# Kernel tuning notes

Hardware: AMD Instinct MI355X
Metric: run time of the kernel (lower is better)

Reference implementation:

```python
import jax, jax.numpy as jnp
import numpy as np

N_NODES = 50000
N_EDGES = 800000
N_LABEL = 200000
IN_DIM = 64
HID = 64
NEG_SLOPE = 0.2  # PyG GATConv default
EPS = 1e-16      # PyG softmax denominator eps


def _gat_conv(x, edge_index, edge_attr, W, att_src, att_dst, We, att_edge, bias):
    """PyG GATConv, heads=1, concat=True, add_self_loops=False, edge_dim=1."""
    n = x.shape[0]
    h = x @ W  # [N, H]
    src, dst = edge_index[0], edge_index[1]
    # per-edge attention logits
    alpha = (h @ att_src)[src] + (h @ att_dst)[dst] + (edge_attr @ We) @ att_edge  # [E]
    alpha = jax.nn.leaky_relu(alpha, NEG_SLOPE)
    # softmax over incoming edges of each dst node
    amax = jax.ops.segment_max(alpha, dst, num_segments=n)
    p = jnp.exp(alpha - amax[dst])
    denom = jax.ops.segment_sum(p, dst, num_segments=n)
    coef = p / (denom[dst] + EPS)  # [E]
    # weighted scatter-aggregate of source features
    out = jax.ops.segment_sum(h[src] * coef[:, None], dst, num_segments=n)
    return out + bias


def setup_inputs() -> dict:
    key = jax.random.key(0)
    ks = jax.random.split(key, 20)
    s = 0.05
    inp = {
        "x": jax.random.normal(ks[0], (N_NODES, IN_DIM), dtype=jnp.float32),
        "edge_attr": jax.random.normal(ks[1], (N_EDGES, 1), dtype=jnp.float32),
        "author_W": jax.random.normal(ks[2], (IN_DIM, HID), dtype=jnp.float32) * s,
        "author_b": jnp.zeros((HID,), dtype=jnp.float32),
        "c1_W": jax.random.normal(ks[3], (HID, HID), dtype=jnp.float32) * s,
        "c1_as": jax.random.normal(ks[4], (HID,), dtype=jnp.float32) * s,
        "c1_ad": jax.random.normal(ks[5], (HID,), dtype=jnp.float32) * s,
        "c1_We": jax.random.normal(ks[6], (1, HID), dtype=jnp.float32) * s,
        "c1_ae": jax.random.normal(ks[7], (HID,), dtype=jnp.float32) * s,
        "c1_b": jnp.zeros((HID,), dtype=jnp.float32),
        "c2_W": jax.random.normal(ks[8], (HID, HID), dtype=jnp.float32) * s,
        "c2_as": jax.random.normal(ks[9], (HID,), dtype=jnp.float32) * s,
        "c2_ad": jax.random.normal(ks[10], (HID,), dtype=jnp.float32) * s,
        "c2_We": jax.random.normal(ks[11], (1, HID), dtype=jnp.float32) * s,
        "c2_ae": jax.random.normal(ks[12], (HID,), dtype=jnp.float32) * s,
        "c2_b": jnp.zeros((HID,), dtype=jnp.float32),
        "edge_index": jax.random.randint(ks[13], (2, N_EDGES), 0, N_NODES, dtype=jnp.int32),
        "edge_label_index": jax.random.randint(ks[14], (2, N_LABEL), 0, N_NODES, dtype=jnp.int32),
    }
    return inp


def reference(x, edge_attr, author_W, author_b,
              c1_W, c1_as, c1_ad, c1_We, c1_ae, c1_b,
              c2_W, c2_as, c2_ad, c2_We, c2_ae, c2_b,
              edge_index, edge_label_index):
    h = x @ author_W + author_b                                   # author_lin
    h = jax.nn.relu(_gat_conv(h, edge_index, edge_attr,
                              c1_W, c1_as, c1_ad, c1_We, c1_ae, c1_b))
    h = _gat_conv(h, edge_index, edge_attr,
                  c2_W, c2_as, c2_ad, c2_We, c2_ae, c2_b)
    # edge-wise dot-product classifier
    return (h[edge_label_index[0]] * h[edge_label_index[1]]).sum(axis=-1)
```

## Files before the change

### kernel.cpp

```cpp
#include <hip/hip_runtime.h>

#define N_NODES 50000
#define N_EDGES 800000
#define N_LABEL 200000
#define HID 64
#define SCAN_BLOCKS 196
#define NBKT 196
#define NBLK 391

static const size_t OFF_W1C  = 0;
static const size_t OFF_B1C  = 4096;
static const size_t OFF_CE   = 4160;
static const size_t OFF_H    = 4224;
static const size_t OFF_AGG  = OFF_H    + (size_t)N_NODES * HID;
static const size_t OFF_ASRC = OFF_AGG  + (size_t)N_NODES * HID;
static const size_t OFF_ADST = OFF_ASRC + (size_t)N_NODES;
static const size_t OFF_ROW  = OFF_ADST + (size_t)N_NODES;
static const size_t OFF_CNT  = OFF_ROW  + (size_t)N_NODES + 2;
static const size_t OFF_PACK = OFF_CNT  + (size_t)N_NODES;
static const size_t OFF_BSUM = OFF_PACK + 2 * (size_t)N_EDGES;
static const size_t OFF_CM   = OFF_BSUM + 256;
static const size_t OFF_OM   = OFF_CM   + (size_t)NBKT * NBLK;

__global__ void prep_kernel(const float* __restrict__ Wa, const float* __restrict__ ba,
                            const float* __restrict__ c1W,
                            const float* __restrict__ c1We, const float* __restrict__ c1ae,
                            const float* __restrict__ c2We, const float* __restrict__ c2ae,
                            float* __restrict__ W1c, float* __restrict__ b1c,
                            float* __restrict__ ce) {
    int t = threadIdx.x;
    for (int idx = t; idx < 64 * 64; idx += 256) {
        int i = idx >> 6, j = idx & 63;
        float s = 0.f;
        for (int k = 0; k < 64; ++k) s += Wa[i * 64 + k] * c1W[k * 64 + j];
        W1c[idx] = s;
    }
    if (t < 64) {
        float s = 0.f;
        for (int k = 0; k < 64; ++k) s += ba[k] * c1W[k * 64 + t];
        b1c[t] = s;
    }
    if (t == 64) {
        float s = 0.f;
        for (int k = 0; k < 64; ++k) s += c1We[k] * c1ae[k];
        ce[0] = s;
    }
    if (t == 65) {
        float s = 0.f;
        for (int k = 0; k < 64; ++k) s += c2We[k] * c2ae[k];
        ce[1] = s;
    }
}

__global__ void hist_kernel(const int* __restrict__ ei, int* __restrict__ cnt) {
    int e = blockIdx.x * blockDim.x + threadIdx.x;
    if (e < N_EDGES) atomicAdd(&cnt[ei[N_EDGES + e]], 1);
}

__global__ void block_sum_kernel(const int* __restrict__ cnt, int* __restrict__ bsum) {
    __shared__ int red[256];
    int t = threadIdx.x;
    int i = blockIdx.x * 256 + t;
    red[t] = (i < N_NODES) ? cnt[i] : 0;
    __syncthreads();
    for (int off = 128; off > 0; off >>= 1) {
        if (t < off) red[t] += red[t + off];
        __syncthreads();
    }
    if (t == 0) bsum[blockIdx.x] = red[0];
}

__global__ void scan_bsum_kernel(int* __restrict__ bsum) {
    __shared__ int s[256];
    int t = threadIdx.x;
    int v = (t < SCAN_BLOCKS) ? bsum[t] : 0;
    s[t] = v;
    __syncthreads();
    for (int off = 1; off < 256; off <<= 1) {
        int u = (t >= off) ? s[t - off] : 0;
        __syncthreads();
        s[t] += u;
        __syncthreads();
    }
    if (t < SCAN_BLOCKS) bsum[t] = s[t] - v;
}

__global__ void scan_final_kernel(const int* __restrict__ cnt,
                                  const int* __restrict__ bsum,
                                  int* __restrict__ row_ptr) {
    __shared__ int s[256];
    int t = threadIdx.x;
    int i = blockIdx.x * 256 + t;
    int v = (i < N_NODES) ? cnt[i] : 0;
    s[t] = v;
    __syncthreads();
    for (int off = 1; off < 256; off <<= 1) {
        int u = (t >= off) ? s[t - off] : 0;
        __syncthreads();
        s[t] += u;
        __syncthreads();
    }
    int excl = s[t] - v + bsum[blockIdx.x];
    if (i < N_NODES) row_ptr[i] = excl;
    if (i == N_NODES - 1) row_ptr[N_NODES] = excl + v;
}

__global__ void blkhist_kernel(const int* __restrict__ ei, int* __restrict__ countM) {
    __shared__ int lh[NBKT];
    int t = threadIdx.x, blk = blockIdx.x;
    if (t < NBKT) lh[t] = 0;
    __syncthreads();
    int base = blk * 2048;
#pragma unroll
    for (int i = 0; i < 8; ++i) {
        int e = base + i * 256 + t;
        if (e < N_EDGES) atomicAdd(&lh[ei[N_EDGES + e] >> 8], 1);
    }
    __syncthreads();
    if (t < NBKT) countM[t * NBLK + blk] = lh[t];
}

__global__ void bucket_scan_kernel(const int* __restrict__ countM,
                                   const int* __restrict__ row_ptr,
                                   int* __restrict__ offM) {
    __shared__ int s[256];
    int b = blockIdx.x, t = threadIdx.x;
    int i0 = 2 * t, i1 = 2 * t + 1;
    int c0 = (i0 < NBLK) ? countM[b * NBLK + i0] : 0;
    int c1 = (i1 < NBLK) ? countM[b * NBLK + i1] : 0;
    int own = c0 + c1;
    s[t] = own;
    __syncthreads();
    for (int off = 1; off < 256; off <<= 1) {
        int u = (t >= off) ? s[t - off] : 0;
        __syncthreads();
        s[t] += u;
        __syncthreads();
    }
    int excl = s[t] - own + row_ptr[b * 256];
    if (i0 < NBLK) offM[b * NBLK + i0] = excl;
    if (i1 < NBLK) offM[b * NBLK + i1] = excl + c0;
}

__global__ void partition_kernel(const int* __restrict__ ei,
                                 const float* __restrict__ ea,
                                 const int* __restrict__ offM,
                                 int2* __restrict__ tmp) {
    __shared__ int lcur[NBKT];
    int t = threadIdx.x, blk = blockIdx.x;
    if (t < NBKT) lcur[t] = offM[t * NBLK + blk];
    __syncthreads();
    int base = blk * 2048;
#pragma unroll
    for (int i = 0; i < 8; ++i) {
        int e = base + i * 256 + t;
        if (e < N_EDGES) {
            int d = ei[N_EDGES + e];
            int pos = atomicAdd(&lcur[d >> 8], 1);
            int2 pr; pr.x = (d << 16) | ei[e]; pr.y = __float_as_int(ea[e]);
            tmp[pos] = pr;
        }
    }
}

__global__ void place_kernel(const int2* __restrict__ tmp,
                             const int* __restrict__ row_ptr,
                             int* __restrict__ cnt,
                             int2* __restrict__ pack) {
    int b = blockIdx.x;
    int beg = row_ptr[b * 256];
    int endn = (b + 1) * 256; if (endn > N_NODES) endn = N_NODES;
    int end = row_ptr[endn];
    for (int pos = beg + threadIdx.x; pos < end; pos += blockDim.x) {
        int2 pr = tmp[pos];
        int d = ((unsigned)pr.x) >> 16;
        int old = atomicSub(&cnt[d], 1);
        int slot = row_ptr[d] + old - 1;
        int2 o; o.x = pr.x & 0xFFFF; o.y = pr.y;
        pack[slot] = o;
    }
}

__global__ void gemm_attn_kernel(const float* __restrict__ X,
                                 const float* __restrict__ W,
                                 const float* __restrict__ postb, int has_postb,
                                 const float* __restrict__ avs,
                                 const float* __restrict__ avd,
                                 float* __restrict__ H,
                                 float* __restrict__ Asrc, float* __restrict__ Adst) {
    int lane = threadIdx.x & 63;
    int wid  = __builtin_amdgcn_readfirstlane(threadIdx.x >> 6);
    int gwave  = blockIdx.x * 4 + wid;
    int nwaves = gridDim.x * 4;
    float wcol[64];
#pragma unroll
    for (int k = 0; k < 64; ++k) wcol[k] = W[k * 64 + lane];
    float as_l = avs[lane], ad_l = avd[lane];
    float ob = has_postb ? postb[lane] : 0.f;
    for (int row = gwave; row < N_NODES; row += nwaves) {
        const float4* xr4 = (const float4*)(X + (size_t)row * 64);
        float acc = ob;
#pragma unroll
        for (int i = 0; i < 16; ++i) {
            float4 xq = xr4[i];
            acc = fmaf(xq.x, wcol[4 * i + 0], acc);
            acc = fmaf(xq.y, wcol[4 * i + 1], acc);
            acc = fmaf(xq.z, wcol[4 * i + 2], acc);
            acc = fmaf(xq.w, wcol[4 * i + 3], acc);
        }
        H[(size_t)row * 64 + lane] = acc;
        float s1 = acc * as_l, s2 = acc * ad_l;
#pragma unroll
        for (int off = 32; off > 0; off >>= 1) {
            s1 += __shfl_xor(s1, off);
            s2 += __shfl_xor(s2, off);
        }
        if (lane == 0) { Asrc[row] = s1; Adst[row] = s2; }
    }
}

__global__ void aggregate_csr_kernel(const int* __restrict__ row_ptr,
                                     const int2* __restrict__ pack,
                                     const float* __restrict__ Asrc,
                                     const float* __restrict__ Adst,
                                     const float* __restrict__ cep,
                                     const float* __restrict__ H,
                                     float* __restrict__ Agg,
                                     const float* __restrict__ obias, int do_relu) {
    int t    = threadIdx.x;
    int q    = t & 15;
    int sub  = (t >> 4) & 3;
    int wid  = t >> 6;
    int node = blockIdx.x * 4 + wid;
    if (node >= N_NODES) return;
    float ce = *cep;
    float ad = Adst[node];
    int beg = row_ptr[node], end = row_ptr[node + 1];
    float ax = 0.f, ay = 0.f, az = 0.f, aw = 0.f, accp = 0.f;
    for (int pos = beg + sub; pos < end; pos += 4) {
        int2  pr  = pack[pos];
        int   s   = pr.x;
        float ev  = __int_as_float(pr.y);
        float as_ = Asrc[s];
        float4 hv = *(const float4*)(H + (size_t)s * 64 + q * 4);
        float al = as_ + ad + ev * ce;
        al = al >= 0.f ? al : 0.2f * al;
        float p = __expf(al);
        ax += p * hv.x; ay += p * hv.y; az += p * hv.z; aw += p * hv.w;
        accp += p;
    }
    ax += __shfl_xor(ax, 16); ax += __shfl_xor(ax, 32);
    ay += __shfl_xor(ay, 16); ay += __shfl_xor(ay, 32);
    az += __shfl_xor(az, 16); az += __shfl_xor(az, 32);
    aw += __shfl_xor(aw, 16); aw += __shfl_xor(aw, 32);
    accp += __shfl_xor(accp, 16); accp += __shfl_xor(accp, 32);
    if (sub == 0) {
        float inv = 1.f / (accp + 1e-16f);
        float4 o; o.x = ax * inv; o.y = ay * inv; o.z = az * inv; o.w = aw * inv;
        if (obias) {
            float4 b = ((const float4*)obias)[q];
            o.x += b.x; o.y += b.y; o.z += b.z; o.w += b.w;
            if (do_relu) {
                o.x = fmaxf(o.x, 0.f); o.y = fmaxf(o.y, 0.f);
                o.z = fmaxf(o.z, 0.f); o.w = fmaxf(o.w, 0.f);
            }
        }
        *(float4*)(Agg + (size_t)node * 64 + q * 4) = o;
    }
}

__global__ void classify_kernel(const int* __restrict__ eli,
                                const float* __restrict__ Agg,
                                const float* __restrict__ bias,
                                float* __restrict__ out) {
    int t    = threadIdx.x;
    int q    = t & 15;
    int grp  = (blockIdx.x * blockDim.x + t) >> 4;
    if (grp >= N_LABEL) return;
    int e = grp;
    float4 b = ((const float4*)bias)[q];
    int i = eli[e], j = eli[N_LABEL + e];
    float4 a = ((const float4*)(Agg + (size_t)i * 64))[q];
    float4 c = ((const float4*)(Agg + (size_t)j * 64))[q];
    float s = (a.x + b.x) * (c.x + b.x) + (a.y + b.y) * (c.y + b.y) +
              (a.z + b.z) * (c.z + b.z) + (a.w + b.w) * (c.w + b.w);
#pragma unroll
    for (int off = 8; off > 0; off >>= 1) s += __shfl_xor(s, off);
    if (q == 0) out[e] = s;
}

extern "C" void kernel_launch(void* const* d_in, const int* in_sizes, int n_in,
                              void* d_out, int out_size, void* d_ws, size_t ws_size,
                              hipStream_t stream) {
    const float* x    = (const float*)d_in[0];
    const float* ea   = (const float*)d_in[1];
    const float* Wa   = (const float*)d_in[2];
    const float* ba   = (const float*)d_in[3];
    const float* c1W  = (const float*)d_in[4];
    const float* c1as = (const float*)d_in[5];
    const float* c1ad = (const float*)d_in[6];
    const float* c1We = (const float*)d_in[7];
    const float* c1ae = (const float*)d_in[8];
    const float* c1b  = (const float*)d_in[9];
    const float* c2W  = (const float*)d_in[10];
    const float* c2as = (const float*)d_in[11];
    const float* c2ad = (const float*)d_in[12];
    const float* c2We = (const float*)d_in[13];
    const float* c2ae = (const float*)d_in[14];
    const float* c2b  = (const float*)d_in[15];
    const int*   ei   = (const int*)d_in[16];
    const int*   eli  = (const int*)d_in[17];
    float* out = (float*)d_out;

    float* w    = (float*)d_ws;
    float* W1c  = w + OFF_W1C;
    float* b1c  = w + OFF_B1C;
    float* ce   = w + OFF_CE;
    float* H    = w + OFF_H;
    float* Agg  = w + OFF_AGG;
    float* Asrc = w + OFF_ASRC;
    float* Adst = w + OFF_ADST;
    int*   rowp = (int*)(w + OFF_ROW);
    int*   cnt  = (int*)(w + OFF_CNT);
    int2*  pack = (int2*)(w + OFF_PACK);
    int*   bsum = (int*)(w + OFF_BSUM);
    int*   cm   = (int*)(w + OFF_CM);
    int*   om   = (int*)(w + OFF_OM);
    int2*  tmp  = (int2*)(w + OFF_H);

    prep_kernel<<<1, 256, 0, stream>>>(Wa, ba, c1W, c1We, c1ae, c2We, c2ae,
                                       W1c, b1c, ce);
    hipMemsetAsync(cnt, 0, (size_t)N_NODES * sizeof(int), stream);
    hist_kernel<<<(N_EDGES + 255) / 256, 256, 0, stream>>>(ei, cnt);
    block_sum_kernel<<<SCAN_BLOCKS, 256, 0, stream>>>(cnt, bsum);
    scan_bsum_kernel<<<1, 256, 0, stream>>>(bsum);
    scan_final_kernel<<<SCAN_BLOCKS, 256, 0, stream>>>(cnt, bsum, rowp);
    blkhist_kernel<<<NBLK, 256, 0, stream>>>(ei, cm);
    bucket_scan_kernel<<<NBKT, 256, 0, stream>>>(cm, rowp, om);
    partition_kernel<<<NBLK, 256, 0, stream>>>(ei, ea, om, tmp);
    place_kernel<<<NBKT, 256, 0, stream>>>(tmp, rowp, cnt, pack);

    gemm_attn_kernel<<<1024, 256, 0, stream>>>(x, W1c, b1c, 1,
                                               c1as, c1ad, H, Asrc, Adst);
    aggregate_csr_kernel<<<12500, 256, 0, stream>>>(rowp, pack, Asrc, Adst,
                                                    ce + 0, H, Agg, c1b, 1);

    gemm_attn_kernel<<<1024, 256, 0, stream>>>(Agg, c2W, nullptr, 0,
                                               c2as, c2ad, H, Asrc, Adst);
    aggregate_csr_kernel<<<12500, 256, 0, stream>>>(rowp, pack, Asrc, Adst,
                                                    ce + 1, H, Agg, nullptr, 0);

    classify_kernel<<<(N_LABEL * 16 + 255) / 256, 256, 0, stream>>>(eli, Agg, c2b, out);
}
```

Baseline: 323.8 us.

## Derive CSR row pointers from bucket partition, drop global histogram and scan kernels

Removes the global per-node histogram, the three-kernel prefix scan and the memset. Bucket bases are now computed inside bucket_scan from the per-block bucket counts, and row_ptr is built per bucket with a shared-memory degree histogram and scan inside the place kernel, which also uses shared-memory cursors instead of global atomics. The weight-folding prep work is merged into block 0 of the histogram kernel. This cuts five launches and one pass of global atomics over the edges. In exchange, bucket_scan redundantly re-sums earlier bucket rows in every block, and block 0 of the histogram kernel takes longer.

```diff
diff --git a/kernel.cpp b/kernel.cpp
--- a/kernel.cpp
+++ b/kernel.cpp
@@ -4,7 +4,6 @@
 #define N_EDGES 800000
 #define N_LABEL 200000
 #define HID 64
-#define SCAN_BLOCKS 196
 #define NBKT 196
 #define NBLK 391
 
@@ -16,96 +15,18 @@
 static const size_t OFF_ASRC = OFF_AGG  + (size_t)N_NODES * HID;
 static const size_t OFF_ADST = OFF_ASRC + (size_t)N_NODES;
 static const size_t OFF_ROW  = OFF_ADST + (size_t)N_NODES;
-static const size_t OFF_CNT  = OFF_ROW  + (size_t)N_NODES + 2;
-static const size_t OFF_PACK = OFF_CNT  + (size_t)N_NODES;
-static const size_t OFF_BSUM = OFF_PACK + 2 * (size_t)N_EDGES;
-static const size_t OFF_CM   = OFF_BSUM + 256;
+static const size_t OFF_PACK = OFF_ROW  + (size_t)N_NODES + 2;
+static const size_t OFF_CM   = OFF_PACK + 2 * (size_t)N_EDGES;
 static const size_t OFF_OM   = OFF_CM   + (size_t)NBKT * NBLK;
-
-__global__ void prep_kernel(const float* __restrict__ Wa, const float* __restrict__ ba,
-                            const float* __restrict__ c1W,
-                            const float* __restrict__ c1We, const float* __restrict__ c1ae,
-                            const float* __restrict__ c2We, const float* __restrict__ c2ae,
-                            float* __restrict__ W1c, float* __restrict__ b1c,
-                            float* __restrict__ ce) {
-    int t = threadIdx.x;
-    for (int idx = t; idx < 64 * 64; idx += 256) {
-        int i = idx >> 6, j = idx & 63;
-        float s = 0.f;
-        for (int k = 0; k < 64; ++k) s += Wa[i * 64 + k] * c1W[k * 64 + j];
-        W1c[idx] = s;
-    }
-    if (t < 64) {
-        float s = 0.f;
-        for (int k = 0; k < 64; ++k) s += ba[k] * c1W[k * 64 + t];
-        b1c[t] = s;
-    }
-    if (t == 64) {
-        float s = 0.f;
-        for (int k = 0; k < 64; ++k) s += c1We[k] * c1ae[k];
-        ce[0] = s;
-    }
-    if (t == 65) {
-        float s = 0.f;
-        for (int k = 0; k < 64; ++k) s += c2We[k] * c2ae[k];
-        ce[1] = s;
-    }
-}
-
-__global__ void hist_kernel(const int* __restrict__ ei, int* __restrict__ cnt) {
-    int e = blockIdx.x * blockDim.x + threadIdx.x;
-    if (e < N_EDGES) atomicAdd(&cnt[ei[N_EDGES + e]], 1);
-}
-
-__global__ void block_sum_kernel(const int* __restrict__ cnt, int* __restrict__ bsum) {
-    __shared__ int red[256];
-    int t = threadIdx.x;
-    int i = blockIdx.x * 256 + t;
-    red[t] = (i < N_NODES) ? cnt[i] : 0;
-    __syncthreads();
-    for (int off = 128; off > 0; off >>= 1) {
-        if (t < off) red[t] += red[t + off];
-        __syncthreads();
-    }
-    if (t == 0) bsum[blockIdx.x] = red[0];
-}
-
-__global__ void scan_bsum_kernel(int* __restrict__ bsum) {
-    __shared__ int s[256];
-    int t = threadIdx.x;
-    int v = (t < SCAN_BLOCKS) ? bsum[t] : 0;
-    s[t] = v;
-    __syncthreads();
-    for (int off = 1; off < 256; off <<= 1) {
-        int u = (t >= off) ? s[t - off] : 0;
-        __syncthreads();
-        s[t] += u;
-        __syncthreads();
-    }
-    if (t < SCAN_BLOCKS) bsum[t] = s[t] - v;
-}
-
-__global__ void scan_final_kernel(const int* __restrict__ cnt,
-                                  const int* __restrict__ bsum,
-                                  int* __restrict__ row_ptr) {
-    __shared__ int s[256];
-    int t = threadIdx.x;
-    int i = blockIdx.x * 256 + t;
-    int v = (i < N_NODES) ? cnt[i] : 0;
-    s[t] = v;
-    __syncthreads();
-    for (int off = 1; off < 256; off <<= 1) {
-        int u = (t >= off) ? s[t - off] : 0;
-        __syncthreads();
-        s[t] += u;
-        __syncthreads();
-    }
-    int excl = s[t] - v + bsum[blockIdx.x];
-    if (i < N_NODES) row_ptr[i] = excl;
-    if (i == N_NODES - 1) row_ptr[N_NODES] = excl + v;
-}
-
-__global__ void blkhist_kernel(const int* __restrict__ ei, int* __restrict__ countM) {
+static const size_t OFF_BKB  = OFF_OM   + (size_t)NBKT * NBLK;
+
+__global__ void blkhist_prep_kernel(const int* __restrict__ ei, int* __restrict__ countM,
+                                    const float* __restrict__ Wa, const float* __restrict__ ba,
+                                    const float* __restrict__ c1W,
+                                    const float* __restrict__ c1We, const float* __restrict__ c1ae,
+                                    const float* __restrict__ c2We, const float* __restrict__ c2ae,
+                                    float* __restrict__ W1c, float* __restrict__ b1c,
+                                    float* __restrict__ ce) {
     __shared__ int lh[NBKT];
     int t = threadIdx.x, blk = blockIdx.x;
     if (t < NBKT) lh[t] = 0;
@@ -118,13 +39,51 @@
     }
     __syncthreads();
     if (t < NBKT) countM[t * NBLK + blk] = lh[t];
+    if (blk == 0) {
+        for (int idx = t; idx < 64 * 64; idx += 256) {
+            int i = idx >> 6, j = idx & 63;
+            float s = 0.f;
+            for (int k = 0; k < 64; ++k) s += Wa[i * 64 + k] * c1W[k * 64 + j];
+            W1c[idx] = s;
+        }
+        if (t < 64) {
+            float s = 0.f;
+            for (int k = 0; k < 64; ++k) s += ba[k] * c1W[k * 64 + t];
+            b1c[t] = s;
+        }
+        if (t == 64) {
+            float s = 0.f;
+            for (int k = 0; k < 64; ++k) s += c1We[k] * c1ae[k];
+            ce[0] = s;
+        }
+        if (t == 65) {
+            float s = 0.f;
+            for (int k = 0; k < 64; ++k) s += c2We[k] * c2ae[k];
+            ce[1] = s;
+        }
+    }
 }
 
 __global__ void bucket_scan_kernel(const int* __restrict__ countM,
-                                   const int* __restrict__ row_ptr,
-                                   int* __restrict__ offM) {
+                                   int* __restrict__ offM,
+                                   int* __restrict__ bktbase) {
     __shared__ int s[256];
     int b = blockIdx.x, t = threadIdx.x;
+    int part = 0;
+    for (int j = t; j < b; j += 256) {
+        const int* row = countM + (size_t)j * NBLK;
+        int rs = 0;
+        for (int i = 0; i < NBLK; ++i) rs += row[i];
+        part += rs;
+    }
+    s[t] = part;
+    __syncthreads();
+    for (int off = 128; off > 0; off >>= 1) {
+        if (t < off) s[t] += s[t + off];
+        __syncthreads();
+    }
+    int base = s[0];
+    __syncthreads();
     int i0 = 2 * t, i1 = 2 * t + 1;
     int c0 = (i0 < NBLK) ? countM[b * NBLK + i0] : 0;
     int c1 = (i1 < NBLK) ? countM[b * NBLK + i1] : 0;
@@ -137,9 +96,14 @@
         s[t] += u;
         __syncthreads();
     }
-    int excl = s[t] - own + row_ptr[b * 256];
+    int excl = s[t] - own + base;
     if (i0 < NBLK) offM[b * NBLK + i0] = excl;
     if (i1 < NBLK) offM[b * NBLK + i1] = excl + c0;
+    if (t == 255) {
+        if (b == 0) bktbase[0] = 0;
+        bktbase[b + 1] = base + s[255];
+    }
+    if (t == 0 && b > 0) bktbase[b] = base;
 }
 
 __global__ void partition_kernel(const int* __restrict__ ei,
@@ -163,19 +127,39 @@
     }
 }
 
-__global__ void place_kernel(const int2* __restrict__ tmp,
-                             const int* __restrict__ row_ptr,
-                             int* __restrict__ cnt,
-                             int2* __restrict__ pack) {
-    int b = blockIdx.x;
-    int beg = row_ptr[b * 256];
-    int endn = (b + 1) * 256; if (endn > N_NODES) endn = N_NODES;
-    int end = row_ptr[endn];
-    for (int pos = beg + threadIdx.x; pos < end; pos += blockDim.x) {
+__global__ void place_rowptr_kernel(const int2* __restrict__ tmp,
+                                    const int* __restrict__ bktbase,
+                                    int* __restrict__ row_ptr,
+                                    int2* __restrict__ pack) {
+    __shared__ int deg[256];
+    __shared__ int s[256];
+    __shared__ int cur[256];
+    int b = blockIdx.x, t = threadIdx.x;
+    int beg = bktbase[b], end = bktbase[b + 1];
+    deg[t] = 0;
+    __syncthreads();
+    for (int pos = beg + t; pos < end; pos += 256)
+        atomicAdd(&deg[(((unsigned)tmp[pos].x) >> 16) & 255], 1);
+    __syncthreads();
+    int v = deg[t];
+    s[t] = v;
+    __syncthreads();
+    for (int off = 1; off < 256; off <<= 1) {
+        int u = (t >= off) ? s[t - off] : 0;
+        __syncthreads();
+        s[t] += u;
+        __syncthreads();
+    }
+    int excl = s[t] - v;
+    int node = b * 256 + t;
+    if (node < N_NODES) row_ptr[node] = beg + excl;
+    if (node == N_NODES - 1) row_ptr[N_NODES] = beg + excl + v;
+    cur[t] = beg + excl;
+    __syncthreads();
+    for (int pos = beg + t; pos < end; pos += 256) {
         int2 pr = tmp[pos];
         int d = ((unsigned)pr.x) >> 16;
-        int old = atomicSub(&cnt[d], 1);
-        int slot = row_ptr[d] + old - 1;
+        int slot = atomicAdd(&cur[d & 255], 1);
         int2 o; o.x = pr.x & 0xFFFF; o.y = pr.y;
         pack[slot] = o;
     }
@@ -321,24 +305,18 @@
     float* Asrc = w + OFF_ASRC;
     float* Adst = w + OFF_ADST;
     int*   rowp = (int*)(w + OFF_ROW);
-    int*   cnt  = (int*)(w + OFF_CNT);
     int2*  pack = (int2*)(w + OFF_PACK);
-    int*   bsum = (int*)(w + OFF_BSUM);
     int*   cm   = (int*)(w + OFF_CM);
     int*   om   = (int*)(w + OFF_OM);
+    int*   bkb  = (int*)(w + OFF_BKB);
     int2*  tmp  = (int2*)(w + OFF_H);
 
-    prep_kernel<<<1, 256, 0, stream>>>(Wa, ba, c1W, c1We, c1ae, c2We, c2ae,
-                                       W1c, b1c, ce);
-    hipMemsetAsync(cnt, 0, (size_t)N_NODES * sizeof(int), stream);
-    hist_kernel<<<(N_EDGES + 255) / 256, 256, 0, stream>>>(ei, cnt);
-    block_sum_kernel<<<SCAN_BLOCKS, 256, 0, stream>>>(cnt, bsum);
-    scan_bsum_kernel<<<1, 256, 0, stream>>>(bsum);
-    scan_final_kernel<<<SCAN_BLOCKS, 256, 0, stream>>>(cnt, bsum, rowp);
-    blkhist_kernel<<<NBLK, 256, 0, stream>>>(ei, cm);
-    bucket_scan_kernel<<<NBKT, 256, 0, stream>>>(cm, rowp, om);
+    blkhist_prep_kernel<<<NBLK, 256, 0, stream>>>(ei, cm, Wa, ba, c1W,
+                                                  c1We, c1ae, c2We, c2ae,
+                                                  W1c, b1c, ce);
+    bucket_scan_kernel<<<NBKT, 256, 0, stream>>>(cm, om, bkb);
     partition_kernel<<<NBLK, 256, 0, stream>>>(ei, ea, om, tmp);
-    place_kernel<<<NBKT, 256, 0, stream>>>(tmp, rowp, cnt, pack);
+    place_rowptr_kernel<<<NBKT, 256, 0, stream>>>(tmp, bkb, rowp, pack);
 
     gemm_attn_kernel<<<1024, 256, 0, stream>>>(x, W1c, b1c, 1,
                                                c1as, c1ad, H, Asrc, Adst);
```

After: 276.4 us. -14.6%, faster.
